# Kernel optimization log

Measured on AMD Instinct MI355X. Metric: run time of the kernel, lower is better.

## Reference

```python
import jax, jax.numpy as jnp
import numpy as np
import math

COV_WEIGHT = 1.0
BANDWIDTH_FACTOR = 1.06
SQRT_2PI = math.sqrt(2.0 * math.pi)
EPS_LOG = 1e-8
H_MIN = 1e-4


def setup_inputs() -> dict:
    key = jax.random.key(0)
    activity = jax.random.normal(key, (2048, 64), dtype=jnp.float32)
    return {"activity": activity}


def reference(activity):
    B, R = activity.shape
    # Silverman bandwidth per receptor (torch .std uses ddof=1)
    std = jnp.std(activity, axis=0, ddof=1)                     # (R,)
    h = jnp.maximum(BANDWIDTH_FACTOR * std * (B ** (-0.2)), H_MIN)  # (R,)

    # Pairwise Gaussian KDE: query == samples == activity
    u = (activity[:, None, :] - activity[None, :, :]) / h       # (B_q, B_s, R)
    kernel_values = jnp.exp(-0.5 * u * u) / SQRT_2PI             # (B_q, B_s, R)
    density = kernel_values.sum(axis=1) / (B * h)                # (B_q, R)

    entropies = -jnp.mean(jnp.log(density + EPS_LOG), axis=0)    # (R,)
    loss_entropy = -entropies.mean()

    # Covariance penalty: sum of squared off-diagonals
    centered = activity - activity.mean(axis=0, keepdims=True)
    cov = (centered.T @ centered) / (B - 1)                      # (R, R)
    off = cov - jnp.diag(jnp.diag(cov))
    loss_cov = jnp.sum(off * off)

    total_loss = loss_entropy + COV_WEIGHT * loss_cov
    return total_loss
```

## Files before the change

### kernel.cpp

```cpp
#include <hip/hip_runtime.h>
#include <math.h>

#define B_SZ 2048
#define R_SZ 64
#define QT 4
#define CH 128
#define NCHUNK (B_SZ / CH)
#define KDE_BLOCKS (B_SZ / QT)

#define B_POW_NEG02 0.217637640824031f
#define SQRT_2PI 2.5066282746310002f
#define LOG2E 1.44269504088896340736f

extern "C" __device__ float __ocml_native_exp2_f32(float);


__global__ __launch_bounds__(1024) void cov_stats_kernel(const float* __restrict__ A,
                                                         float* __restrict__ U,
                                                         float* __restrict__ lscale,
                                                         float* __restrict__ cov_partial,
                                                         float* __restrict__ ent_acc,
                                                         int* __restrict__ done_cnt) {
    int i = blockIdx.x;
    int tid = threadIdx.x;
    int j = tid & 63, bg = tid >> 6;

    float g = 0.f, sj = 0.f, s2j = 0.f;
#pragma unroll 4
    for (int b = bg; b < B_SZ; b += 16) {
        float ai = A[b * R_SZ + i];
        float aj = A[b * R_SZ + j];
        g = fmaf(ai, aj, g);
        sj += aj;
        s2j = fmaf(aj, aj, s2j);
    }

    __shared__ float gred[16][64], sred[16][64], s2red[16][64];
    __shared__ float gfin[64], sfin[64], hs[64];
    gred[bg][j] = g; sred[bg][j] = sj; s2red[bg][j] = s2j;
    __syncthreads();
    if (tid < 64) {
        float G = 0.f, S = 0.f, S2 = 0.f;
#pragma unroll
        for (int t = 0; t < 16; ++t) { G += gred[t][j]; S += sred[t][j]; S2 += s2red[t][j]; }
        gfin[j] = G;
        sfin[j] = S;
        float m = S * (1.f / (float)B_SZ);
        float var = (S2 - S * m) * (1.f / (float)(B_SZ - 1));
        var = fmaxf(var, 0.f);
        float h = fmaxf(1.06f * sqrtf(var) * B_POW_NEG02, 1e-4f);
        hs[j] = sqrtf(0.5f * LOG2E) / h;
        if (i == 0) lscale[j] = 1.0f / ((float)B_SZ * h * SQRT_2PI);
    }
    __syncthreads();
    if (tid < 64) {
        float m_j = sfin[j] * (1.f / (float)B_SZ);
        float m_i = sfin[i] * (1.f / (float)B_SZ);
        float cov = (gfin[j] - (float)B_SZ * m_i * m_j) * (1.f / (float)(B_SZ - 1));
        float v = (j == i) ? 0.f : cov * cov;
        for (int off = 32; off > 0; off >>= 1) v += __shfl_down(v, off, 64);
        if (j == 0) cov_partial[i] = v;
    }
    if (i == 0 && tid == 64) { *ent_acc = 0.f; *done_cnt = 0; }

    int base = i * (32 * R_SZ);
    float k0 = hs[tid & 63];
    U[base + tid]        = A[base + tid]        * k0;
    U[base + 1024 + tid] = A[base + 1024 + tid] * k0;
}

__global__ __launch_bounds__(1024) void kde_kernel(const float* __restrict__ U,
                                                   const float* __restrict__ lscale,
                                                   const float* __restrict__ cov_partial,
                                                   float* __restrict__ ent_acc,
                                                   int* __restrict__ done_cnt,
                                                   float* __restrict__ out) {
    __shared__ float Us[CH * R_SZ];
    int tid = threadIdx.x;
    int r = tid & 63, sg = tid >> 6;
    int q0 = blockIdx.x * QT;

    float uq0 = U[(q0 + 0) * R_SZ + r];
    float uq1 = U[(q0 + 1) * R_SZ + r];
    float uq2 = U[(q0 + 2) * R_SZ + r];
    float uq3 = U[(q0 + 3) * R_SZ + r];
    float c0 = 0.f, c1 = 0.f, c2 = 0.f, c3 = 0.f;

    for (int ch = 0; ch < NCHUNK; ++ch) {
        const float4* src = (const float4*)(U + ch * (CH * R_SZ));
        float4* dst = (float4*)Us;
        dst[tid]        = src[tid];
        dst[tid + 1024] = src[tid + 1024];
        __syncthreads();
#pragma unroll
        for (int it = 0; it < CH / 16; ++it) {
            float us = Us[(sg + 16 * it) * R_SZ + r];
            float d0 = uq0 - us; c0 += __ocml_native_exp2_f32(-d0 * d0);
            float d1 = uq1 - us; c1 += __ocml_native_exp2_f32(-d1 * d1);
            float d2 = uq2 - us; c2 += __ocml_native_exp2_f32(-d2 * d2);
            float d3 = uq3 - us; c3 += __ocml_native_exp2_f32(-d3 * d3);
        }
        __syncthreads();
    }

    float (*red)[QT][64] = (float (*)[QT][64])Us;
    red[sg][0][r] = c0;
    red[sg][1][r] = c1;
    red[sg][2][r] = c2;
    red[sg][3][r] = c3;
    __syncthreads();
    __shared__ float wred[QT];
    if (sg < QT) {
        float S = 0.f;
#pragma unroll
        for (int t = 0; t < 16; ++t) S += red[t][sg][r];
        float v = __logf(fmaf(S, lscale[r], 1e-8f));
        for (int off = 32; off > 0; off >>= 1) v += __shfl_down(v, off, 64);
        if (r == 0) wred[sg] = v;
    }
    __syncthreads();
    __shared__ int lastflag;
    if (tid == 0) {
        float p = (wred[0] + wred[1] + wred[2] + wred[3]) *
                  (1.0f / ((float)B_SZ * (float)R_SZ));
        atomicAdd(ent_acc, p);
        __threadfence();
        int prev = atomicAdd(done_cnt, 1);
        lastflag = (prev == KDE_BLOCKS - 1);
    }
    __syncthreads();
    if (lastflag && tid < 64) {
        __threadfence();
        float v = cov_partial[tid];
        for (int off = 32; off > 0; off >>= 1) v += __shfl_down(v, off, 64);
        if (tid == 0) {
            float ent = __hip_atomic_load(ent_acc, __ATOMIC_ACQUIRE,
                                          __HIP_MEMORY_SCOPE_AGENT);
            out[0] = ent + v;
        }
    }
}

extern "C" void kernel_launch(void* const* d_in, const int* in_sizes, int n_in,
                              void* d_out, int out_size, void* d_ws, size_t ws_size,
                              hipStream_t stream) {
    const float* A = (const float*)d_in[0];
    float* out = (float*)d_out;

    float* wsf = (float*)d_ws;
    float* lscale      = wsf;
    float* cov_partial = wsf + 64;
    float* ent_acc     = wsf + 160;
    int*   done_cnt    = (int*)(wsf + 192);
    float* U           = wsf + 256;

    cov_stats_kernel<<<R_SZ, 1024, 0, stream>>>(A, U, lscale, cov_partial,
                                                ent_acc, done_cnt);
    kde_kernel<<<KDE_BLOCKS, 1024, 0, stream>>>(U, lscale, cov_partial,
                                                ent_acc, done_cnt, out);
}
```

Measured before the change: 108.6 us.

## Read KDE samples directly from global memory with packed float2 math

Removes the shared-memory staging of sample chunks and the two barriers per chunk in the KDE kernel. Each thread now streams its sample values straight from global memory, relying on the L2 and L1 caches since U is small. The per-pair subtract, square and accumulate are written on two-wide float vectors so the compiler can emit packed FP32 instructions. This trades LDS reuse and explicit synchronisation for more global/cache load traffic per block.

Result: no change. 107.0 us (-1.5%).

```diff
diff --git a/kernel.cpp b/kernel.cpp
--- a/kernel.cpp
+++ b/kernel.cpp
@@ -4,8 +4,6 @@
 #define B_SZ 2048
 #define R_SZ 64
 #define QT 4
-#define CH 128
-#define NCHUNK (B_SZ / CH)
 #define KDE_BLOCKS (B_SZ / QT)
 
 #define B_POW_NEG02 0.217637640824031f
@@ -13,6 +11,8 @@
 #define LOG2E 1.44269504088896340736f
 
 extern "C" __device__ float __ocml_native_exp2_f32(float);
+
+typedef __attribute__((ext_vector_type(2))) float f32x2;
 
 
 __global__ __launch_bounds__(1024) void cov_stats_kernel(const float* __restrict__ A,
@@ -75,39 +75,33 @@
                                                    float* __restrict__ ent_acc,
                                                    int* __restrict__ done_cnt,
                                                    float* __restrict__ out) {
-    __shared__ float Us[CH * R_SZ];
     int tid = threadIdx.x;
     int r = tid & 63, sg = tid >> 6;
     int q0 = blockIdx.x * QT;
 
-    float uq0 = U[(q0 + 0) * R_SZ + r];
-    float uq1 = U[(q0 + 1) * R_SZ + r];
-    float uq2 = U[(q0 + 2) * R_SZ + r];
-    float uq3 = U[(q0 + 3) * R_SZ + r];
-    float c0 = 0.f, c1 = 0.f, c2 = 0.f, c3 = 0.f;
+    f32x2 uq01 = { U[(q0 + 0) * R_SZ + r], U[(q0 + 1) * R_SZ + r] };
+    f32x2 uq23 = { U[(q0 + 2) * R_SZ + r], U[(q0 + 3) * R_SZ + r] };
+    f32x2 c01 = { 0.f, 0.f }, c23 = { 0.f, 0.f };
 
-    for (int ch = 0; ch < NCHUNK; ++ch) {
-        const float4* src = (const float4*)(U + ch * (CH * R_SZ));
-        float4* dst = (float4*)Us;
-        dst[tid]        = src[tid];
-        dst[tid + 1024] = src[tid + 1024];
-        __syncthreads();
-#pragma unroll
-        for (int it = 0; it < CH / 16; ++it) {
-            float us = Us[(sg + 16 * it) * R_SZ + r];
-            float d0 = uq0 - us; c0 += __ocml_native_exp2_f32(-d0 * d0);
-            float d1 = uq1 - us; c1 += __ocml_native_exp2_f32(-d1 * d1);
-            float d2 = uq2 - us; c2 += __ocml_native_exp2_f32(-d2 * d2);
-            float d3 = uq3 - us; c3 += __ocml_native_exp2_f32(-d3 * d3);
-        }
-        __syncthreads();
+#pragma unroll 4
+    for (int s = sg; s < B_SZ; s += 16) {
+        float us = U[s * R_SZ + r];
+        f32x2 uss = { us, us };
+        f32x2 d01 = uq01 - uss;
+        f32x2 d23 = uq23 - uss;
+        f32x2 n01 = -d01 * d01;
+        f32x2 n23 = -d23 * d23;
+        f32x2 e01 = { __ocml_native_exp2_f32(n01.x), __ocml_native_exp2_f32(n01.y) };
+        f32x2 e23 = { __ocml_native_exp2_f32(n23.x), __ocml_native_exp2_f32(n23.y) };
+        c01 += e01;
+        c23 += e23;
     }
 
-    float (*red)[QT][64] = (float (*)[QT][64])Us;
-    red[sg][0][r] = c0;
-    red[sg][1][r] = c1;
-    red[sg][2][r] = c2;
-    red[sg][3][r] = c3;
+    __shared__ float red[16][QT][64];
+    red[sg][0][r] = c01.x;
+    red[sg][1][r] = c01.y;
+    red[sg][2][r] = c23.x;
+    red[sg][3][r] = c23.y;
     __syncthreads();
     __shared__ float wred[QT];
     if (sg < QT) {
```
